# Kernel tuning notes

Measured on AMD Instinct MI355X. Metric: run time of the kernel, lower is better.

The kernel has to match this reference:

```python
import jax, jax.numpy as jnp
import numpy as np
import math

B, T, D = 2, 4096, 2048
H, d_head, C = 16, 128, 64


def binarize(x):
    # sign to {-1,+1} with straight-through estimator (identity gradient)
    s = jnp.where(x >= 0, jnp.ones_like(x), -jnp.ones_like(x))
    return x + jax.lax.stop_gradient(s - x)


def setup_inputs() -> dict:
    key = jax.random.key(0)
    ks = jax.random.split(key, 5)
    w_std = 1.0 / math.sqrt(D)
    return {
        "x": jax.random.normal(ks[0], (B, T, D), dtype=jnp.float32),
        "Wq": jax.random.normal(ks[1], (D, D), dtype=jnp.float32) * w_std,
        "Wk": jax.random.normal(ks[2], (D, D), dtype=jnp.float32) * w_std,
        "Wv": jax.random.normal(ks[3], (D, D), dtype=jnp.float32) * w_std,
        "Wo": jax.random.normal(ks[4], (D, D), dtype=jnp.float32) * w_std,
    }


def reference(x, Wq, Wk, Wv, Wo):
    Bx, Tx, Dx = x.shape
    scale = 1.0 / math.sqrt(d_head)
    # projections (torch Linear: y = x @ W.T), split heads -> [B,H,T,d]
    q = (x @ Wq.T).reshape(Bx, Tx, H, d_head).transpose(0, 2, 1, 3) * scale
    k = binarize((x @ Wk.T).reshape(Bx, Tx, H, d_head).transpose(0, 2, 1, 3))
    v = binarize((x @ Wv.T).reshape(Bx, Tx, H, d_head).transpose(0, 2, 1, 3))
    N = Tx // C  # T chosen divisible by chunk_size
    qc = q.reshape(Bx, H, N, C, d_head)
    kc = k.reshape(Bx, H, N, C, d_head)
    vc = v.reshape(Bx, H, N, C, d_head)
    # intra-chunk causal attention
    mask = jnp.tril(jnp.ones((C, C), dtype=x.dtype))
    intra_scores = jnp.einsum('bhnid,bhnjd->bhnij', qc, kc) * mask
    intra = jnp.einsum('bhnij,bhnjd->bhnid', intra_scores, vc)
    # cross-chunk: exclusive prefix sum of per-chunk k^T v outer products
    chunk_kv = jnp.einsum('bhnci,bhncj->bhnij', kc, vc)  # [B,H,N,d,d]
    cs = jnp.cumsum(chunk_kv, axis=2)
    prefix = cs - chunk_kv  # exclusive cumsum
    cross = jnp.einsum('bhncd,bhnde->bhnce', qc, prefix)
    output = (intra + cross).reshape(Bx, H, Tx, d_head)
    out = output.transpose(0, 2, 1, 3).reshape(Bx, Tx, Dx) @ Wo.T
    final_state = cs[:, :, -1]  # [B,H,d,d]
    return out, final_state
```

## Files before the change

kernel.cpp:

```cpp
#include <hip/hip_runtime.h>
#include <stdint.h>

typedef __attribute__((ext_vector_type(8))) short short8;
typedef __attribute__((ext_vector_type(4))) float f32x4;
typedef unsigned short u16;

__device__ __forceinline__ u16 f2bf(float f) {
  uint32_t u = __builtin_bit_cast(uint32_t, f);
  u = (u + 0x7FFFu + ((u >> 16) & 1u)) >> 16;
  return (u16)u;
}
__device__ __forceinline__ float bf2f(u16 h) {
  uint32_t u = ((uint32_t)h) << 16;
  return __builtin_bit_cast(float, u);
}
__device__ __forceinline__ void lds16(const u16* g, u16* l) {
  __builtin_amdgcn_global_load_lds(
      (const __attribute__((address_space(1))) void*)g,
      (__attribute__((address_space(3))) void*)l, 16, 0, 0);
}
__device__ __forceinline__ int sw256(int i) { return i ^ (((i >> 7) & 7) << 3); }
__device__ __forceinline__ int sw128(int i) { return i ^ (((i >> 6) & 7) << 3); }
__device__ __forceinline__ int swzA64(int i) { return i ^ (((i >> 6) & 7) << 3); }
__device__ __forceinline__ int swzA32(int i) { return i ^ (((i >> 6) & 3) << 3); }

#define SB0() __builtin_amdgcn_sched_barrier(0)
#define BAR() __builtin_amdgcn_s_barrier()
#define LGKM0() do { asm volatile("s_waitcnt lgkmcnt(0)" ::: "memory"); SB0(); } while (0)
#define VM(n) asm volatile("s_waitcnt vmcnt(" #n ")" ::: "memory")
#define VMNOP do {} while (0)

__global__ void split_kernel(const float* __restrict__ in, u16* __restrict__ hi,
                             u16* __restrict__ lo, int n) {
  int i = blockIdx.x * blockDim.x + threadIdx.x;
  int stride = gridDim.x * blockDim.x;
  for (; i < n; i += stride) {
    float v = in[i];
    u16 h = f2bf(v);
    hi[i] = h;
    if (lo) lo[i] = f2bf(v - bf2f(h));
  }
}

template<int SPLIT, int EPI>
__global__ __launch_bounds__(512, 2) void gemm8p(
    const u16* __restrict__ Ahi, const u16* __restrict__ Alo,
    const u16* __restrict__ Bhi, const u16* __restrict__ Blo,
    u16* __restrict__ outb, float* __restrict__ outf,
    int Mdim, int Ndim, int Kdim)
{
  constexpr int BK   = (SPLIT > 1) ? 32 : 64;
  constexpr int TILE = 256 * BK;
  constexpr int NMAT = (SPLIT > 1) ? 4 : 2;
  constexpr int AOFF_H = 0;
  constexpr int AOFF_L = (SPLIT > 1) ? TILE : 0;
  constexpr int BOFF_H = (SPLIT > 1) ? 2*TILE : TILE;
  constexpr int BOFF_L = (SPLIT > 1) ? 3*TILE : 0;
  __shared__ __align__(16) u16 smem[2 * NMAT * TILE];

  const int t = threadIdx.x, l = t & 63;
  const int w = t >> 6;
  const int wm = w >> 2, wn = w & 3;
  const int fr = l & 15, fs = l >> 4;
  const int sb = (blockIdx.x & 7) * 32 + (blockIdx.x >> 3);
  const int m0 = (sb >> 3) * 256, n0 = (sb & 7) * 256;
  const int NT = Kdim / BK;

  auto ST = [&](const u16* src, int g0, int moff, int kt, int r) {
    if (kt >= NT) return;
    const int bufb = (kt & 1) * NMAT * TILE;
    int d = r * 4096 + t * 8;
    int row, scol;
    if constexpr (SPLIT == 1) { row = d >> 6; scol = ((d >> 3) & 7) ^ (row & 7); }
    else                      { row = d >> 5; scol = ((d >> 3) & 3) ^ ((row >> 1) & 3); }
    lds16(src + (size_t)(g0 + row) * Kdim + kt * BK + scol * 8,
          smem + bufb + moff + d);
  };

  f32x4 acc[8][4] = {};

#define SWZ(i) ((BK == 64) ? swzA64(i) : swzA32(i))
  auto RD8 = [&](short8* dst, int bufb, int off) {
#pragma unroll
    for (int fm = 0; fm < 8; fm++) {
      int ia = (wm*128 + fm*16 + fr)*BK + fs*8;
      dst[fm] = *(const short8*)(smem + bufb + off + SWZ(ia));
    }
  };
  auto RD4 = [&](short8* dst, int bufb, int off) {
#pragma unroll
    for (int fn = 0; fn < 4; fn++) {
      int ib = (wn*64 + fn*16 + fr)*BK + fs*8;
      dst[fn] = *(const short8*)(smem + bufb + off + SWZ(ib));
    }
  };
  auto RDQ = [&](short8* dst, int bufb, int q) {
#pragma unroll
    for (int i = 0; i < 2; i++)
#pragma unroll
      for (int ks = 0; ks < 2; ks++) {
        int ia = (wm*128 + (2*q+i)*16 + fr)*64 + ks*32 + fs*8;
        dst[i*2+ks] = *(const short8*)(smem + bufb + AOFF_H + swzA64(ia));
      }
  };
  auto RDB8 = [&](short8* dst, int bufb) {
#pragma unroll
    for (int fn = 0; fn < 4; fn++)
#pragma unroll
      for (int ks = 0; ks < 2; ks++) {
        int ib = (wn*64 + fn*16 + fr)*64 + ks*32 + fs*8;
        dst[fn*2+ks] = *(const short8*)(smem + bufb + BOFF_H + swzA64(ib));
      }
  };

#define PASS32(RA, RB) do {                                                    \
  __builtin_amdgcn_s_setprio(1);                                               \
  _Pragma("unroll") for (int fm_ = 0; fm_ < 8; fm_++)                          \
    _Pragma("unroll") for (int fn_ = 0; fn_ < 4; fn_++)                        \
      acc[fm_][fn_] = __builtin_amdgcn_mfma_f32_16x16x32_bf16(                 \
          (RA)[fm_], (RB)[fn_], acc[fm_][fn_], 0, 0, 0);                       \
  __builtin_amdgcn_s_setprio(0);                                               \
  SB0();                                                                       \
} while (0)

#define PASS16(Q, AQ, BB) do {                                                 \
  __builtin_amdgcn_s_setprio(1);                                               \
  _Pragma("unroll") for (int i_ = 0; i_ < 2; i_++)                             \
    _Pragma("unroll") for (int fn_ = 0; fn_ < 4; fn_++)                        \
      _Pragma("unroll") for (int ks_ = 0; ks_ < 2; ks_++)                      \
        acc[2*(Q)+i_][fn_] = __builtin_amdgcn_mfma_f32_16x16x32_bf16(          \
            (AQ)[i_*2+ks_], (BB)[fn_*2+ks_], acc[2*(Q)+i_][fn_], 0, 0, 0);     \
  __builtin_amdgcn_s_setprio(0);                                               \
  SB0();                                                                       \
} while (0)

#define T3BODY(T, W0, W1, W2) {                                                \
  const int bufb = ((T) & 1) * NMAT * TILE;                                    \
  short8 xah[8], xbh[4], xbl[4], xal[8];                                       \
  RD8(xah, bufb, AOFF_H); RD4(xbh, bufb, BOFF_H);                              \
  ST(Ahi, m0, AOFF_H, (T)+1, 0); ST(Ahi, m0, AOFF_H, (T)+1, 1);                \
  ST(Bhi, n0, BOFF_H, (T)+1, 0); ST(Bhi, n0, BOFF_H, (T)+1, 1);                \
  W0; BAR(); LGKM0(); PASS32(xah, xbh); BAR();                                 \
  RD4(xbl, bufb, BOFF_L);                                                      \
  ST(Blo, n0, BOFF_L, (T)+1, 0); ST(Blo, n0, BOFF_L, (T)+1, 1);                \
  W1; BAR(); LGKM0(); PASS32(xah, xbl); BAR();                                 \
  RD8(xal, bufb, AOFF_L);                                                      \
  ST(Alo, m0, AOFF_L, (T)+1, 0); ST(Alo, m0, AOFF_L, (T)+1, 1);                \
  W2; BAR(); LGKM0(); PASS32(xal, xbh); BAR();                                 \
}

#define T1BODY(T, W1, W3) {                                                    \
  const int bufb = ((T) & 1) * NMAT * TILE;                                    \
  short8 bb[8], aq[4];                                                         \
  RDB8(bb, bufb); RDQ(aq, bufb, 0);                                            \
  ST(Bhi, n0, BOFF_H, (T)+1, 0); ST(Bhi, n0, BOFF_H, (T)+1, 1);                \
  BAR(); LGKM0(); PASS16(0, aq, bb); BAR();                                    \
  RDQ(aq, bufb, 1);                                                            \
  ST(Bhi, n0, BOFF_H, (T)+1, 2); ST(Bhi, n0, BOFF_H, (T)+1, 3);                \
  W1; BAR(); LGKM0(); PASS16(1, aq, bb); BAR();                                \
  RDQ(aq, bufb, 2);                                                            \
  ST(Ahi, m0, AOFF_H, (T)+1, 0); ST(Ahi, m0, AOFF_H, (T)+1, 2);                \
  BAR(); LGKM0(); PASS16(2, aq, bb); BAR();                                    \
  RDQ(aq, bufb, 3);                                                            \
  ST(Ahi, m0, AOFF_H, (T)+1, 1); ST(Ahi, m0, AOFF_H, (T)+1, 3);                \
  W3; BAR(); LGKM0(); PASS16(3, aq, bb); BAR();                                \
}

  if constexpr (SPLIT > 1) {
    ST(Ahi, m0, AOFF_H, 0, 0); ST(Ahi, m0, AOFF_H, 0, 1);
    ST(Bhi, n0, BOFF_H, 0, 0); ST(Bhi, n0, BOFF_H, 0, 1);
    ST(Blo, n0, BOFF_L, 0, 0); ST(Blo, n0, BOFF_L, 0, 1);
    ST(Alo, m0, AOFF_L, 0, 0); ST(Alo, m0, AOFF_L, 0, 1);
    VM(4); BAR();
    for (int T = 0; T < NT - 1; T++) T3BODY(T, VM(6), VM(6), VM(4))
    T3BODY(NT - 1, VM(2), VM(0), VMNOP)
  } else {
    ST(Bhi, n0, BOFF_H, 0, 0); ST(Bhi, n0, BOFF_H, 0, 1);
    ST(Bhi, n0, BOFF_H, 0, 2); ST(Bhi, n0, BOFF_H, 0, 3);
    ST(Ahi, m0, AOFF_H, 0, 0); ST(Ahi, m0, AOFF_H, 0, 2);
    ST(Ahi, m0, AOFF_H, 0, 1); ST(Ahi, m0, AOFF_H, 0, 3);
    VM(2); BAR();
    for (int T = 0; T < NT - 1; T++) T1BODY(T, VM(4), VM(2))
    T1BODY(NT - 1, VM(0), VMNOP)
  }
#undef SWZ
#undef T3BODY
#undef T1BODY
#undef PASS32
#undef PASS16

  const float qscale = 0.08838834764831843f;
#pragma unroll
  for (int fm = 0; fm < 8; fm++)
#pragma unroll
    for (int fn = 0; fn < 4; fn++)
#pragma unroll
      for (int r = 0; r < 4; r++) {
        int gm = m0 + wm*128 + fm*16 + fs*4 + r;
        int gn = n0 + wn*64 + fn*16 + fr;
        float val = acc[fm][fn][r];
        if constexpr (EPI == 2) {
          outf[(size_t)gm * Ndim + gn] = val;
        } else {
          int b = gm >> 12, tt = gm & 4095, h = gn >> 7, dd = gn & 127;
          size_t idx = (((size_t)(b*16 + h))*4096 + tt)*128 + dd;
          if constexpr (EPI == 0) outb[idx] = f2bf(val * qscale);
          else                    outb[idx] = (val >= 0.f) ? (u16)0x3F80 : (u16)0xBF80;
        }
      }
}

__global__ void pack_signs(const u16* __restrict__ k, const u16* __restrict__ v,
                           unsigned long long* __restrict__ kp, unsigned long long* __restrict__ vp) {
  const int blk = blockIdx.x;
  const int d = threadIdx.x;
  const int bh = blk >> 6, n = blk & 63;
  size_t base = (((size_t)bh * 4096) + n * 64) * 128 + d;
  unsigned long long kw = 0, vw = 0;
  for (int c = 0; c < 64; c++) {
    kw |= (unsigned long long)(k[base + (size_t)c*128] >> 15) << c;
    vw |= (unsigned long long)(v[base + (size_t)c*128] >> 15) << c;
  }
  kp[(size_t)blk * 128 + d] = kw;
  vp[(size_t)blk * 128 + d] = vw;
}

__global__ __launch_bounds__(256) void scan_kernel(
    const unsigned long long* __restrict__ kp, const unsigned long long* __restrict__ vp,
    short* __restrict__ pfx8, float* __restrict__ fsT)
{
  const int t = threadIdx.x;
  const int bh = blockIdx.x >> 6, ep = blockIdx.x & 63;
  const int e = ep * 2 + (t >> 7), d = t & 127;
  const size_t base = (size_t)bh * 64 * 128;
  int s = 0;
  for (int n = 0; n < 64; n++) {
    if ((n & 7) == 0)
      pfx8[((size_t)(bh*8 + (n>>3))*128 + e)*128 + d] = (short)s;
    unsigned long long kw = kp[base + (size_t)n*128 + d];
    unsigned long long vw = vp[base + (size_t)n*128 + e];
    s += 64 - 2*__popcll(kw ^ vw);
  }
  fsT[((size_t)bh*128 + e)*128 + d] = (float)s;
}

__global__ __launch_bounds__(256) void transpose_fs(const float* __restrict__ fsT,
                                                    float* __restrict__ fstate) {
  __shared__ float tile[32*130];
  const int t = threadIdx.x;
  const int bh = blockIdx.x >> 2, es = (blockIdx.x & 3) * 32;
#pragma unroll
  for (int i = 0; i < 16; i++) {
    int idx = t + i*256;
    int e2 = idx >> 7, d = idx & 127;
    tile[e2*130 + d] = fsT[((size_t)bh*128 + es + e2)*128 + d];
  }
  __syncthreads();
#pragma unroll
  for (int i = 0; i < 16; i++) {
    int idx = t + i*256;
    int d = idx >> 5, e2 = idx & 31;
    fstate[((size_t)bh*128 + d)*128 + es + e2] = tile[e2*130 + d];
  }
}

__global__ __launch_bounds__(256) void fused_attn(
    const u16* __restrict__ q, const u16* __restrict__ k,
    const unsigned long long* __restrict__ kp, const unsigned long long* __restrict__ vp,
    const short* __restrict__ pfx8, u16* __restrict__ att)
{
  __shared__ __align__(16) u16 smem[28672];
  u16* sQ  = smem;
  u16* sP1 = smem + 8192;
  u16* sP2 = smem + 16384;
  u16* sS  = smem + 24576;

  const int t = threadIdx.x, l = t & 63, w = t >> 6;
  const int blk = blockIdx.x, bh = blk >> 6, n = blk & 63;
  const int b = bh >> 4, hh = bh & 15;
  const int fr = l & 15, fs = l >> 4;
  const size_t qbase = (((size_t)bh * 4096) + n * 64) * 128;
  const size_t pbase = (size_t)bh * 64 * 128;

#pragma unroll
  for (int i = 0; i < 4; i++) {
    int arow = i*16 + (t>>4);
    int aslot = (t & 15) ^ (arow & 7);
    size_t g = qbase + (size_t)arow*128 + aslot*8;
    lds16(q + g, sQ + i*2048 + t*8);
    lds16(k + g, sP1 + i*2048 + t*8);
  }
  {
    int d = t >> 1, ch = (t & 1) * 32;
    unsigned long long wv = vp[pbase + (size_t)n*128 + d];
#pragma unroll
    for (int c = 0; c < 32; c += 2) {
      uint32_t b0 = ((wv >> (ch + c)) & 1ull)     ? 0xBF80u : 0x3F80u;
      uint32_t b1 = ((wv >> (ch + c + 1)) & 1ull) ? 0xBF80u : 0x3F80u;
      int li = d*64 + ch + c;
      *(uint32_t*)(sP2 + sw128(li)) = b0 | (b1 << 16);
    }
  }
  __syncthreads();

  f32x4 accS[4] = {};
#pragma unroll
  for (int kk = 0; kk < 4; kk++) {
    int la = (w*16 + fr)*128 + kk*32 + fs*8;
    short8 a = *(const short8*)(sQ + sw256(la));
#pragma unroll
    for (int fn = 0; fn < 4; fn++) {
      int lb = (fn*16 + fr)*128 + kk*32 + fs*8;
      short8 bb = *(const short8*)(sP1 + sw256(lb));
      accS[fn] = __builtin_amdgcn_mfma_f32_16x16x32_bf16(a, bb, accS[fn], 0, 0, 0);
    }
  }
#pragma unroll
  for (int fn = 0; fn < 4; fn++)
#pragma unroll
    for (int r = 0; r < 4; r++) {
      int i = w*16 + fs*4 + r, j = fn*16 + fr;
      float v = (j <= i) ? accS[fn][r] : 0.f;
      sS[sw128(i*64 + j)] = f2bf(v);
    }
  __syncthreads();

  f32x4 accI[8] = {};
#pragma unroll
  for (int kk = 0; kk < 2; kk++) {
    int la = (w*16 + fr)*64 + kk*32 + fs*8;
    short8 a = *(const short8*)(sS + sw128(la));
#pragma unroll
    for (int fn = 0; fn < 8; fn++) {
      int lb = (fn*16 + fr)*64 + kk*32 + fs*8;
      short8 bb = *(const short8*)(sP2 + sw128(lb));
      accI[fn] = __builtin_amdgcn_mfma_f32_16x16x32_bf16(a, bb, accI[fn], 0, 0, 0);
    }
  }
  __syncthreads();

  const int m0 = n & ~7, cnt = n & 7;
  for (int hf = 0; hf < 2; hf++) {
#pragma unroll
    for (int p = 0; p < 4; p++) {
      int erow = p*16 + (t>>4);
      int e = hf*64 + erow;
      const short* ps = pfx8 + ((size_t)(bh*8 + (n>>3))*128 + e)*128 + (t&15)*8;
      short8 pv = *(const short8*)ps;
      int accj[8];
#pragma unroll
      for (int j = 0; j < 8; j++) accj[j] = pv[j];
      for (int m = 0; m < cnt; m++) {
        unsigned long long vw = vp[pbase + (size_t)(m0+m)*128 + e];
#pragma unroll
        for (int j = 0; j < 8; j++) {
          unsigned long long kw = kp[pbase + (size_t)(m0+m)*128 + (t&15)*8 + j];
          accj[j] += 64 - 2*__popcll(kw ^ vw);
        }
      }
      short8 hi, lo;
#pragma unroll
      for (int j = 0; j < 8; j++) {
        hi[j] = (short)f2bf((float)(accj[j] >> 5));
        lo[j] = (short)f2bf((float)(accj[j] & 31));
      }
      int pi = sw256(erow*128 + (t&15)*8);
      *(short8*)(sP1 + pi) = hi;
      *(short8*)(sP2 + pi) = lo;
    }
    __syncthreads();

    f32x4 acch[4] = {}, accl[4] = {};
#pragma unroll
    for (int kk = 0; kk < 4; kk++) {
      int la = (w*16 + fr)*128 + kk*32 + fs*8;
      short8 a = *(const short8*)(sQ + sw256(la));
#pragma unroll
      for (int fn = 0; fn < 4; fn++) {
        int pb = sw256((fn*16 + fr)*128 + kk*32 + fs*8);
        acch[fn] = __builtin_amdgcn_mfma_f32_16x16x32_bf16(a, *(const short8*)(sP1 + pb), acch[fn], 0, 0, 0);
        accl[fn] = __builtin_amdgcn_mfma_f32_16x16x32_bf16(a, *(const short8*)(sP2 + pb), accl[fn], 0, 0, 0);
      }
    }
#pragma unroll
    for (int fn = 0; fn < 4; fn++)
#pragma unroll
      for (int r = 0; r < 4; r++) {
        int c = w*16 + fs*4 + r;
        int dcol = hf*64 + fn*16 + fr;
        float val = accI[hf*4+fn][r] + 32.f*acch[fn][r] + accl[fn][r];
        size_t idx = ((size_t)(b*4096 + n*64 + c))*2048 + hh*128 + dcol;
        att[idx] = f2bf(val);
      }
    __syncthreads();
  }
}

extern "C" void kernel_launch(void* const* d_in, const int* in_sizes, int n_in,
                              void* d_out, int out_size, void* d_ws, size_t ws_size,
                              hipStream_t stream) {
  (void)in_sizes; (void)n_in; (void)out_size; (void)ws_size;
  const float* x  = (const float*)d_in[0];
  const float* Wq = (const float*)d_in[1];
  const float* Wk = (const float*)d_in[2];
  const float* Wv = (const float*)d_in[3];
  const float* Wo = (const float*)d_in[4];
  float* out = (float*)d_out;
  float* fstate = out + (size_t)16777216;

  char* ws = (char*)d_ws;
  u16* x_hi = (u16*)(ws + 0);
  u16* x_lo = (u16*)(ws + 33554432);
  u16* qb   = (u16*)(ws + 67108864);
  u16* kb   = (u16*)(ws + 100663296);
  u16* vb   = (u16*)(ws + 134217728);
  u16* wq_h = (u16*)(ws + 167772160);
  u16* wk_h = (u16*)(ws + 176160768);
  u16* wk_l = (u16*)(ws + 184549376);
  u16* wv_h = (u16*)(ws + 192937984);
  u16* wv_l = (u16*)(ws + 201326592);
  u16* wo_h = (u16*)(ws + 209715200);
  unsigned long long* kpk = (unsigned long long*)(ws + 218103808);
  unsigned long long* vpk = (unsigned long long*)(ws + 220200960);
  u16* att    = x_hi;
  float* fsT  = (float*)(ws + 33554432);
  short* pfx8 = (short*)(ws + 134217728);

  split_kernel<<<2048, 256, 0, stream>>>(x,  x_hi, x_lo, 16777216);
  split_kernel<<<1024, 256, 0, stream>>>(Wq, wq_h, nullptr, 4194304);
  split_kernel<<<1024, 256, 0, stream>>>(Wk, wk_h, wk_l, 4194304);
  split_kernel<<<1024, 256, 0, stream>>>(Wv, wv_h, wv_l, 4194304);
  split_kernel<<<1024, 256, 0, stream>>>(Wo, wo_h, nullptr, 4194304);

  gemm8p<1,0><<<256, 512, 0, stream>>>(x_hi, nullptr, wq_h, nullptr, qb, nullptr, 8192, 2048, 2048);
  gemm8p<3,1><<<256, 512, 0, stream>>>(x_hi, x_lo, wk_h, wk_l, kb, nullptr, 8192, 2048, 2048);
  gemm8p<3,1><<<256, 512, 0, stream>>>(x_hi, x_lo, wv_h, wv_l, vb, nullptr, 8192, 2048, 2048);

  pack_signs<<<2048, 128, 0, stream>>>(kb, vb, kpk, vpk);
  scan_kernel<<<2048, 256, 0, stream>>>(kpk, vpk, pfx8, fsT);
  transpose_fs<<<128, 256, 0, stream>>>(fsT, fstate);
  fused_attn<<<2048, 256, 0, stream>>>(qb, kb, kpk, vpk, pfx8, att);

  gemm8p<1,2><<<256, 512, 0, stream>>>(att, nullptr, wo_h, nullptr, nullptr, out, 8192, 2048, 2048);
}
```

Baseline: 683.4 us.

## Restructure GEMM main loop with register-prefetched fragments and one barrier per tile

Replaces the per-sub-pass barrier scheme in both GEMM variants with a loop that loads all LDS fragments for a tile up front. It uses partial lgkmcnt waits so the MFMA passes start as their fragments arrive, and keeps a single barrier per K-tile. Global-to-LDS loads for tile T+2 are issued after that barrier, and the first fragment of the next tile is read before the final MFMA pass. This is meant to cut barrier and wait stalls and overlap LDS reads with matrix math. The cost is many more live fragment registers alongside the 128-float accumulator, which under the 512-thread, 2-block launch bound may cause spills or lower occupancy.

```diff
diff --git a/kernel.cpp b/kernel.cpp
--- a/kernel.cpp
+++ b/kernel.cpp
@@ -26,9 +26,8 @@
 
 #define SB0() __builtin_amdgcn_sched_barrier(0)
 #define BAR() __builtin_amdgcn_s_barrier()
-#define LGKM0() do { asm volatile("s_waitcnt lgkmcnt(0)" ::: "memory"); SB0(); } while (0)
+#define LGKM(n) do { asm volatile("s_waitcnt lgkmcnt(" #n ")" ::: "memory"); SB0(); } while (0)
 #define VM(n) asm volatile("s_waitcnt vmcnt(" #n ")" ::: "memory")
-#define VMNOP do {} while (0)
 
 __global__ void split_kernel(const float* __restrict__ in, u16* __restrict__ hi,
                              u16* __restrict__ lo, int n) {
@@ -76,6 +75,19 @@
     lds16(src + (size_t)(g0 + row) * Kdim + kt * BK + scol * 8,
           smem + bufb + moff + d);
   };
+  auto ST8 = [&](int kt) {
+    if constexpr (SPLIT == 1) {
+      ST(Bhi, n0, BOFF_H, kt, 0); ST(Bhi, n0, BOFF_H, kt, 1);
+      ST(Bhi, n0, BOFF_H, kt, 2); ST(Bhi, n0, BOFF_H, kt, 3);
+      ST(Ahi, m0, AOFF_H, kt, 0); ST(Ahi, m0, AOFF_H, kt, 1);
+      ST(Ahi, m0, AOFF_H, kt, 2); ST(Ahi, m0, AOFF_H, kt, 3);
+    } else {
+      ST(Ahi, m0, AOFF_H, kt, 0); ST(Ahi, m0, AOFF_H, kt, 1);
+      ST(Bhi, n0, BOFF_H, kt, 0); ST(Bhi, n0, BOFF_H, kt, 1);
+      ST(Blo, n0, BOFF_L, kt, 0); ST(Blo, n0, BOFF_L, kt, 1);
+      ST(Alo, m0, AOFF_L, kt, 0); ST(Alo, m0, AOFF_L, kt, 1);
+    }
+  };
 
   f32x4 acc[8][4] = {};
 
@@ -123,7 +135,7 @@
   SB0();                                                                       \
 } while (0)
 
-#define PASS16(Q, AQ, BB) do {                                                 \
+#define PASS16Q(Q, AQ, BB) do {                                                \
   __builtin_amdgcn_s_setprio(1);                                               \
   _Pragma("unroll") for (int i_ = 0; i_ < 2; i_++)                             \
     _Pragma("unroll") for (int fn_ = 0; fn_ < 4; fn_++)                        \
@@ -134,60 +146,50 @@
   SB0();                                                                       \
 } while (0)
 
-#define T3BODY(T, W0, W1, W2) {                                                \
-  const int bufb = ((T) & 1) * NMAT * TILE;                                    \
-  short8 xah[8], xbh[4], xbl[4], xal[8];                                       \
-  RD8(xah, bufb, AOFF_H); RD4(xbh, bufb, BOFF_H);                              \
-  ST(Ahi, m0, AOFF_H, (T)+1, 0); ST(Ahi, m0, AOFF_H, (T)+1, 1);                \
-  ST(Bhi, n0, BOFF_H, (T)+1, 0); ST(Bhi, n0, BOFF_H, (T)+1, 1);                \
-  W0; BAR(); LGKM0(); PASS32(xah, xbh); BAR();                                 \
-  RD4(xbl, bufb, BOFF_L);                                                      \
-  ST(Blo, n0, BOFF_L, (T)+1, 0); ST(Blo, n0, BOFF_L, (T)+1, 1);                \
-  W1; BAR(); LGKM0(); PASS32(xah, xbl); BAR();                                 \
-  RD8(xal, bufb, AOFF_L);                                                      \
-  ST(Alo, m0, AOFF_L, (T)+1, 0); ST(Alo, m0, AOFF_L, (T)+1, 1);                \
-  W2; BAR(); LGKM0(); PASS32(xal, xbh); BAR();                                 \
-}
-
-#define T1BODY(T, W1, W3) {                                                    \
-  const int bufb = ((T) & 1) * NMAT * TILE;                                    \
-  short8 bb[8], aq[4];                                                         \
-  RDB8(bb, bufb); RDQ(aq, bufb, 0);                                            \
-  ST(Bhi, n0, BOFF_H, (T)+1, 0); ST(Bhi, n0, BOFF_H, (T)+1, 1);                \
-  BAR(); LGKM0(); PASS16(0, aq, bb); BAR();                                    \
-  RDQ(aq, bufb, 1);                                                            \
-  ST(Bhi, n0, BOFF_H, (T)+1, 2); ST(Bhi, n0, BOFF_H, (T)+1, 3);                \
-  W1; BAR(); LGKM0(); PASS16(1, aq, bb); BAR();                                \
-  RDQ(aq, bufb, 2);                                                            \
-  ST(Ahi, m0, AOFF_H, (T)+1, 0); ST(Ahi, m0, AOFF_H, (T)+1, 2);                \
-  BAR(); LGKM0(); PASS16(2, aq, bb); BAR();                                    \
-  RDQ(aq, bufb, 3);                                                            \
-  ST(Ahi, m0, AOFF_H, (T)+1, 1); ST(Ahi, m0, AOFF_H, (T)+1, 3);                \
-  W3; BAR(); LGKM0(); PASS16(3, aq, bb); BAR();                                \
-}
-
   if constexpr (SPLIT > 1) {
-    ST(Ahi, m0, AOFF_H, 0, 0); ST(Ahi, m0, AOFF_H, 0, 1);
-    ST(Bhi, n0, BOFF_H, 0, 0); ST(Bhi, n0, BOFF_H, 0, 1);
-    ST(Blo, n0, BOFF_L, 0, 0); ST(Blo, n0, BOFF_L, 0, 1);
-    ST(Alo, m0, AOFF_L, 0, 0); ST(Alo, m0, AOFF_L, 0, 1);
-    VM(4); BAR();
-    for (int T = 0; T < NT - 1; T++) T3BODY(T, VM(6), VM(6), VM(4))
-    T3BODY(NT - 1, VM(2), VM(0), VMNOP)
+    short8 Ah[8], Al[8], Bh[4], Bl[4];
+    ST8(0); ST8(1);
+    VM(8); BAR();
+    RD8(Ah, 0, AOFF_H);
+    for (int T = 0; T < NT; T++) {
+      const int cb = (T & 1) * NMAT * TILE;
+      const int nb = ((T + 1) & 1) * NMAT * TILE;
+      RD4(Bh, cb, BOFF_H);
+      RD4(Bl, cb, BOFF_L);
+      RD8(Al, cb, AOFF_L);
+      LGKM(12); PASS32(Ah, Bh);
+      LGKM(8);  PASS32(Ah, Bl);
+      LGKM(0); VM(0); BAR();
+      ST8(T + 2);
+      RD8(Ah, nb, AOFF_H);
+      SB0();
+      PASS32(Al, Bh);
+    }
   } else {
-    ST(Bhi, n0, BOFF_H, 0, 0); ST(Bhi, n0, BOFF_H, 0, 1);
-    ST(Bhi, n0, BOFF_H, 0, 2); ST(Bhi, n0, BOFF_H, 0, 3);
-    ST(Ahi, m0, AOFF_H, 0, 0); ST(Ahi, m0, AOFF_H, 0, 2);
-    ST(Ahi, m0, AOFF_H, 0, 1); ST(Ahi, m0, AOFF_H, 0, 3);
-    VM(2); BAR();
-    for (int T = 0; T < NT - 1; T++) T1BODY(T, VM(4), VM(2))
-    T1BODY(NT - 1, VM(0), VMNOP)
+    short8 B[8], a0[4], a1[4], a2[4], a3[4];
+    ST8(0); ST8(1);
+    VM(8); BAR();
+    RDQ(a0, 0, 0);
+    for (int T = 0; T < NT; T++) {
+      const int cb = (T & 1) * NMAT * TILE;
+      const int nb = ((T + 1) & 1) * NMAT * TILE;
+      RDB8(B, cb);
+      RDQ(a1, cb, 1);
+      RDQ(a2, cb, 2);
+      RDQ(a3, cb, 3);
+      LGKM(12); PASS16Q(0, a0, B);
+      LGKM(8);  PASS16Q(1, a1, B);
+      LGKM(4);  PASS16Q(2, a2, B);
+      LGKM(0); VM(0); BAR();
+      ST8(T + 2);
+      RDQ(a0, nb, 0);
+      SB0();
+      PASS16Q(3, a3, B);
+    }
   }
 #undef SWZ
-#undef T3BODY
-#undef T1BODY
 #undef PASS32
-#undef PASS16
+#undef PASS16Q
 
   const float qscale = 0.08838834764831843f;
 #pragma unroll
```

After: 1.269 ms. 1.86x slower.
